# Kernel optimization log

Measured on AMD Instinct MI355X. Metric: run time of the kernel, lower is better.

## Reference

```python
import jax, jax.numpy as jnp
import numpy as np


def setup_inputs() -> dict:
    key = jax.random.key(0)
    k1, k2, k3, k4 = jax.random.split(key, 4)
    B, N, F, H, O = 4, 2048, 256, 8, 256
    nodes = jax.random.normal(k1, (B, N, F), dtype=jnp.float32)
    W_heads = jax.random.normal(k2, (H, F, F), dtype=jnp.float32) * (1.0 / np.sqrt(F))
    W_out = jax.random.normal(k3, (H * F, O), dtype=jnp.float32) * (1.0 / np.sqrt(H * F))
    bias = jax.random.normal(k4, (O,), dtype=jnp.float32) * 0.02
    return {"nodes": nodes, "W_heads": W_heads, "W_out": W_out, "bias": bias}


def reference(nodes, W_heads, W_out, bias):
    # nodes: [B,N,F]; W_heads: [H,F,F]; W_out: [H*F,O]; bias: [O]
    B, N, F = nodes.shape
    H = W_heads.shape[0]
    norm = 1.0 / jnp.sqrt(jnp.asarray(F, dtype=nodes.dtype))
    # per-head bilinear scores: (x @ W_h) @ x^T  -> [B,H,N,N]
    xw = jnp.einsum('bnf,hfg->bhng', nodes, W_heads)
    scores = jnp.einsum('bhng,bmg->bhnm', xw, nodes) * norm
    att = jax.nn.softmax(scores, axis=-1)
    # messages: att @ x (V = input nodes) -> [B,H,N,F]
    msgs = jnp.einsum('bhnm,bmf->bhnf', att, nodes)
    # concat heads along feature axis (head 0 first) -> [B,N,H*F]
    msgs = msgs.transpose(0, 2, 1, 3).reshape(B, N, H * F)
    return jnp.matmul(msgs, W_out) + bias
```

## Files before the change

kernel.cpp:

```cpp
#include <hip/hip_runtime.h>
#include <hip/hip_bf16.h>

#define B_ 4
#define N_ 2048
#define F_ 256
#define H_ 8
#define O_ 256

#define SCALE_QK 0.09016844005556021f

typedef __attribute__((ext_vector_type(8))) short short8;
typedef __attribute__((ext_vector_type(4))) short s16x4;
typedef __attribute__((ext_vector_type(4))) float f32x4;
typedef __attribute__((ext_vector_type(4))) unsigned int u32x4;

static __device__ __forceinline__ float bf2f(short u) {
    unsigned int x = ((unsigned int)(unsigned short)u) << 16;
    return __builtin_bit_cast(float, x);
}
static __device__ __forceinline__ short f2bf(float f) {
    unsigned int x = __builtin_bit_cast(unsigned int, f);
    unsigned int lsb = (x >> 16) & 1u;
    x += 0x7fffu + lsb;
    return (short)(x >> 16);
}
static __device__ __forceinline__ unsigned int cvtpk(float a, float b) {
    unsigned int r;
    asm("v_cvt_pk_bf16_f32 %0, %1, %2" : "=v"(r) : "v"(a), "v"(b));
    return r;
}

static __device__ __forceinline__ void gld16(const short* g, short* l) {
    __builtin_amdgcn_global_load_lds(
        (const __attribute__((address_space(1))) void*)g,
        (__attribute__((address_space(3))) void*)l, 16, 0, 0);
}

__global__ __launch_bounds__(256) void cvtT_kernel(const float* __restrict__ src,
                                                   short* __restrict__ dstT,
                                                   short* __restrict__ dst2,
                                                   int R, int C) {
    __shared__ short tile[32][33];
    src  += (size_t)blockIdx.z * R * C;
    dstT += (size_t)blockIdx.z * R * C;
    if (dst2) dst2 += (size_t)blockIdx.z * R * C;
    int tx = threadIdx.x, ty = threadIdx.y;
    int c0 = blockIdx.x * 32, r0 = blockIdx.y * 32;
#pragma unroll
    for (int j = 0; j < 4; j++) {
        int r = r0 + ty + j * 8;
        short v = f2bf(src[(size_t)r * C + c0 + tx]);
        tile[ty + j * 8][tx] = v;
        if (dst2) dst2[(size_t)r * C + c0 + tx] = v;
    }
    __syncthreads();
#pragma unroll
    for (int j = 0; j < 4; j++) {
        int c = c0 + ty + j * 8;
        dstT[(size_t)c * R + r0 + tx] = tile[tx][ty + j * 8];
    }
}

__global__ __launch_bounds__(512) void out_kernel(const short* __restrict__ msgs,
                                                  const short* __restrict__ WoutT,
                                                  const float* __restrict__ bias,
                                                  float* __restrict__ out) {
    __shared__ short sA[2][64 * 64];
    __shared__ short sB[2][128 * 64];
    int mt = blockIdx.x, nt = blockIdx.y;
    int tid = threadIdx.x, w = tid >> 6, l = tid & 63, lq = l & 15, quad = l >> 4;
    const short* Arow = msgs  + (size_t)(mt * 64)  * (H_ * F_);
    const short* Brow = WoutT + (size_t)(nt * 128) * (H_ * F_);
    int xk = (l & 7) ^ (l >> 3);

    f32x4 acc[4];
#pragma unroll
    for (int i = 0; i < 4; i++) acc[i] = (f32x4)(0.f);

#define STAGE_OUT(KB, BI) do {                                               \
        gld16(&Arow[(size_t)(w * 8 + (l >> 3)) * (H_ * F_) + (KB) * 64 + xk * 8], \
              &sA[BI][w * 8 * 64]);                                          \
        gld16(&Brow[(size_t)(w * 16 + (l >> 3)) * (H_ * F_) + (KB) * 64 + xk * 8], \
              &sB[BI][w * 16 * 64]);                                         \
        gld16(&Brow[(size_t)(w * 16 + 8 + (l >> 3)) * (H_ * F_) + (KB) * 64 + xk * 8], \
              &sB[BI][(w * 16 + 8) * 64]);                                   \
    } while (0)

    STAGE_OUT(0, 0);
    __syncthreads();

#pragma unroll 1
    for (int kb = 0; kb < 32; kb++) {
        int cur = kb & 1;
        if (kb < 31) STAGE_OUT(kb + 1, cur ^ 1);
        int arow = (w & 3) * 16 + lq;
#pragma unroll
        for (int kk = 0; kk < 2; kk++) {
            short8 af = *(const short8*)&sA[cur][arow * 64 + (((kk * 4 + quad) ^ (arow & 7)) * 8)];
#pragma unroll
            for (int ct = 0; ct < 4; ct++) {
                int brow = (w >> 2) * 64 + ct * 16 + lq;
                short8 bf = *(const short8*)&sB[cur][brow * 64 + (((kk * 4 + quad) ^ (brow & 7)) * 8)];
                acc[ct] = __builtin_amdgcn_mfma_f32_16x16x32_bf16(af, bf, acc[ct], 0, 0, 0);
            }
        }
        __syncthreads();
    }

#pragma unroll
    for (int ct = 0; ct < 4; ct++) {
        int gcol = nt * 128 + (w >> 2) * 64 + ct * 16 + lq;
        float bv = bias[gcol];
#pragma unroll
        for (int r = 0; r < 4; r++) {
            int row = mt * 64 + (w & 3) * 16 + quad * 4 + r;
            out[(size_t)row * O_ + gcol] = acc[ct][r] + bv;
        }
    }
}


#define STAGE_KV(KT, KVF, KVTF) do {                                         \
    _Pragma("unroll")                                                        \
    for (int i_ = 0; i_ < 4; i_++) {                                         \
        int rk_ = w * 8 + i_ * 2 + (l >> 5);                                 \
        int bk_ = (l & 31) ^ (rk_ & 31);                                     \
        gld16(&Xb[(size_t)((KT) * 64 + rk_) * F_ + bk_ * 8],                 \
              &KVF[(w * 8 + i_ * 2) * 256]);                                 \
        int rt_ = w * 32 + i_ * 8 + (l >> 3);                                \
        int bt_ = (l & 7) ^ (rt_ & 7);                                       \
        gld16(&XTb[(size_t)rt_ * N_ + (KT) * 64 + bt_ * 8],                  \
              &KVTF[(w * 32 + i_ * 8) * 64]);                                \
    }                                                                        \
} while (0)

#define COMPUTE_KT(KVF, KVTF) do {                                           \
    f32x4 sacc[4];                                                           \
    _Pragma("unroll")                                                        \
    for (int ct = 0; ct < 4; ct++) sacc[ct] = (f32x4)(0.f);                  \
    __builtin_amdgcn_s_setprio(1);                                           \
    _Pragma("unroll")                                                        \
    for (int kk = 0; kk < 8; kk++) {                                         \
        _Pragma("unroll")                                                    \
        for (int ct = 0; ct < 4; ct++) {                                     \
            int arow = ct * 16 + lq;                                         \
            int ab = (kk * 4 + quad) ^ (arow & 31);                          \
            short8 af = *(const short8*)&KVF[arow * 256 + ab * 8];           \
            sacc[ct] = __builtin_amdgcn_mfma_f32_16x16x32_bf16(af, aq[kk], sacc[ct], 0, 0, 0); \
        }                                                                    \
    }                                                                        \
    __builtin_amdgcn_s_setprio(0);                                           \
    float mx = -INFINITY;                                                    \
    _Pragma("unroll")                                                        \
    for (int ct = 0; ct < 4; ct++)                                           \
        _Pragma("unroll")                                                    \
        for (int r_ = 0; r_ < 4; r_++) mx = fmaxf(mx, sacc[ct][r_]);         \
    mx = fmaxf(mx, __shfl_xor(mx, 16));                                      \
    mx = fmaxf(mx, __shfl_xor(mx, 32));                                      \
    if (!__all(mx - m_q <= 8.0f)) {                \
        float mn = fmaxf(m_q, mx);                                           \
        float alpha = exp2f(m_q - mn);                                       \
        m_q = mn;                                                            \
        l_q *= alpha;                                                        \
        _Pragma("unroll")                                                    \
        for (int ct = 0; ct < 16; ct++)                                      \
            _Pragma("unroll")                                                \
            for (int r_ = 0; r_ < 4; r_++) oacc[ct][r_] *= alpha;            \
    }                                                                        \
    float pv[4][4]; float s_ = 0.f;                                          \
    _Pragma("unroll")                                                        \
    for (int ct = 0; ct < 4; ct++)                                           \
        _Pragma("unroll")                                                    \
        for (int r_ = 0; r_ < 4; r_++) {                                     \
            pv[ct][r_] = exp2f(sacc[ct][r_] - m_q);                          \
            s_ += pv[ct][r_];                                                \
        }                                                                    \
    s_ += __shfl_xor(s_, 16);                                                \
    s_ += __shfl_xor(s_, 32);                                                \
    l_q += s_;                                                               \
    unsigned int w2[4][2];                                                   \
    _Pragma("unroll")                                                        \
    for (int ct = 0; ct < 4; ct++) {                                         \
        w2[ct][0] = cvtpk(pv[ct][0], pv[ct][1]);                             \
        w2[ct][1] = cvtpk(pv[ct][2], pv[ct][3]);                             \
    }                                                                        \
    int sl0 = (2 * (quad & 1)) * 16 + lq;                                    \
    int sl1 = sl0 + 16;                                                      \
    bool hi = (quad >> 1) != 0;                                              \
    short8 pfrag[2];                                                         \
    _Pragma("unroll")                                                        \
    for (int kk = 0; kk < 2; kk++) {                                         \
        unsigned int u0 = __shfl((int)w2[2 * kk][0], sl0);                   \
        unsigned int u1 = __shfl((int)w2[2 * kk][1], sl0);                   \
        unsigned int u2 = __shfl((int)w2[2 * kk][0], sl1);                   \
        unsigned int u3 = __shfl((int)w2[2 * kk][1], sl1);                   \
        unsigned int v0 = __shfl((int)w2[2 * kk + 1][0], sl0);               \
        unsigned int v1 = __shfl((int)w2[2 * kk + 1][1], sl0);               \
        unsigned int v2 = __shfl((int)w2[2 * kk + 1][0], sl1);               \
        unsigned int v3 = __shfl((int)w2[2 * kk + 1][1], sl1);               \
        u32x4 pk = { hi ? v0 : u0, hi ? v1 : u1, hi ? v2 : u2, hi ? v3 : u3 }; \
        pfrag[kk] = __builtin_bit_cast(short8, pk);                          \
    }                                                                        \
    __builtin_amdgcn_s_setprio(1);                                           \
    _Pragma("unroll")                                                        \
    for (int ct = 0; ct < 16; ct++) {                                        \
        int arow = ct * 16 + lq;                                             \
        short8 a0 = *(const short8*)&KVTF[arow * 64 + ((quad) ^ (arow & 7)) * 8]; \
        short8 a1 = *(const short8*)&KVTF[arow * 64 + ((4 + quad) ^ (arow & 7)) * 8]; \
        oacc[ct] = __builtin_amdgcn_mfma_f32_16x16x32_bf16(a0, pfrag[0], oacc[ct], 0, 0, 0); \
        oacc[ct] = __builtin_amdgcn_mfma_f32_16x16x32_bf16(a1, pfrag[1], oacc[ct], 0, 0, 0); \
    }                                                                        \
    __builtin_amdgcn_s_setprio(0);                                           \
} while (0)

__global__ __launch_bounds__(512) void attn_kernel(const short* __restrict__ X,
                                                   const short* __restrict__ WhT,
                                                   const short* __restrict__ XT,
                                                   short* __restrict__ msgs) {
    __shared__ short kvfA[64 * 256];
    __shared__ short kvfB[64 * 256];
    __shared__ short kvTfA[256 * 64];
    __shared__ short kvTfB[256 * 64];

    int qt = blockIdx.x, bh = blockIdx.y, b = bh >> 3, h = bh & 7;
    int tid = threadIdx.x, w = tid >> 6, l = tid & 63, lq = l & 15, quad = l >> 4;
    int q0 = qt * 128;

    const short* Xb  = X  + (size_t)b * N_ * F_;
    const short* XTb = XT + (size_t)b * F_ * N_;
    const short* Whh = WhT + (size_t)h * F_ * F_;

    f32x4 oacc[16];
    short8 aq[8];

#pragma unroll
    for (int i = 0; i < 16; i++) oacc[i] = (f32x4)(0.f);
    {
        short* xdst = (w < 4) ? kvfA : kvfB;
        int wl = w & 3;
#pragma unroll
        for (int i = 0; i < 8; i++) {
            int r = wl * 16 + i * 2 + (l >> 5);
            int bb = (l & 31) ^ (r & 31);
            gld16(&Xb[(size_t)(q0 + ((w >> 2) * 64) + r) * F_ + bb * 8],
                  &xdst[(wl * 16 + i * 2) * 256]);
        }
    }
    const short* xsrc = (w < 4) ? kvfA : kvfB;
#pragma unroll 1
    for (int kb = 0; kb < 4; kb++) {
        __syncthreads();
#pragma unroll
        for (int i = 0; i < 4; i++) {
            int rt = w * 32 + i * 8 + (l >> 3);
            int bt = (l & 7) ^ (rt & 7);
            gld16(&Whh[(size_t)rt * F_ + kb * 64 + bt * 8], &kvTfA[(w * 32 + i * 8) * 64]);
        }
        __syncthreads();
#pragma unroll
        for (int kk = 0; kk < 2; kk++) {
            int arow = (w & 3) * 16 + lq;
            int ab = (kb * 8 + kk * 4 + quad) ^ (arow & 31);
            short8 af = *(const short8*)&xsrc[arow * 256 + ab * 8];
#pragma unroll
            for (int ct = 0; ct < 16; ct++) {
                int brow = ct * 16 + lq;
                int bb = (kk * 4 + quad) ^ (brow & 7);
                short8 bf = *(const short8*)&kvTfA[brow * 64 + bb * 8];
                oacc[ct] = __builtin_amdgcn_mfma_f32_16x16x32_bf16(af, bf, oacc[ct], 0, 0, 0);
            }
        }
    }
    __syncthreads();
    {
        short* qdst = (w < 4) ? kvTfA : kvTfB;
#pragma unroll
        for (int ct = 0; ct < 16; ct++) {
#pragma unroll
            for (int r = 0; r < 4; r++) {
                int row = (w & 3) * 16 + quad * 4 + r;
                int col = ct * 16 + lq;
                int pb = (col >> 3) ^ (row & 31);
                qdst[row * 256 + pb * 8 + (col & 7)] = f2bf(oacc[ct][r] * SCALE_QK);
            }
        }
        __syncthreads();
#pragma unroll
        for (int kk = 0; kk < 8; kk++) {
            int row = (w & 3) * 16 + lq;
            int ab = (kk * 4 + quad) ^ (row & 31);
            aq[kk] = *(const short8*)&qdst[row * 256 + ab * 8];
        }
    }
    __syncthreads();

#pragma unroll
    for (int i = 0; i < 16; i++) oacc[i] = (f32x4)(0.f);
    float m_q = -INFINITY, l_q = 0.f;

    STAGE_KV(0, kvfA, kvTfA);
    __syncthreads();

#pragma unroll 1
    for (int kt2 = 0; kt2 < 16; kt2++) {
        STAGE_KV(2 * kt2 + 1, kvfB, kvTfB);
        COMPUTE_KT(kvfA, kvTfA);
        __syncthreads();
        STAGE_KV((2 * kt2 + 2) & 31, kvfA, kvTfA);
        COMPUTE_KT(kvfB, kvTfB);
        __syncthreads();
    }

    float inv = 1.f / l_q;
    short* Mout = msgs + (size_t)(b * N_ + q0 + w * 16 + lq) * (H_ * F_) + h * F_;
#pragma unroll
    for (int ct = 0; ct < 16; ct++) {
        s16x4 v4 = { f2bf(oacc[ct][0] * inv), f2bf(oacc[ct][1] * inv),
                     f2bf(oacc[ct][2] * inv), f2bf(oacc[ct][3] * inv) };
        *(s16x4*)&Mout[ct * 16 + quad * 4] = v4;
    }
}

extern "C" void kernel_launch(void* const* d_in, const int* in_sizes, int n_in,
                              void* d_out, int out_size, void* d_ws, size_t ws_size,
                              hipStream_t stream) {
    const float* nodes = (const float*)d_in[0];
    const float* Wh    = (const float*)d_in[1];
    const float* Wout  = (const float*)d_in[2];
    const float* bias  = (const float*)d_in[3];
    float* out = (float*)d_out;

    char* ws = (char*)d_ws;
    short* msgs   = (short*)(ws);
    short* WhT    = (short*)(ws + 33554432);
    short* WoutT  = (short*)(ws + 34603008);
    short* XT     = (short*)(ws + 35651584);
    short* Xbf    = (short*)(ws + 39845888);

    dim3 tblk(32, 8, 1);
    hipLaunchKernelGGL(cvtT_kernel, dim3(8, 8, 8),  tblk, 0, stream, Wh,    WhT,   (short*)nullptr, 256,  256);
    hipLaunchKernelGGL(cvtT_kernel, dim3(8, 64, 1), tblk, 0, stream, Wout,  WoutT, (short*)nullptr, 2048, 256);
    hipLaunchKernelGGL(cvtT_kernel, dim3(8, 64, 4), tblk, 0, stream, nodes, XT,    Xbf,             2048, 256);

    hipLaunchKernelGGL(attn_kernel, dim3(16, 32), dim3(512), 0, stream, Xbf, WhT, XT, msgs);
    hipLaunchKernelGGL(out_kernel,  dim3(128, 2), dim3(512), 0, stream, msgs, WoutT, bias, out);
}
```

Before: 289.0 us.

## Double attention block to 16 waves covering 256 query rows per workgroup

```diff
diff --git a/kernel.cpp b/kernel.cpp
--- a/kernel.cpp
+++ b/kernel.cpp
@@ -122,15 +122,15 @@
 
 #define STAGE_KV(KT, KVF, KVTF) do {                                         \
     _Pragma("unroll")                                                        \
-    for (int i_ = 0; i_ < 4; i_++) {                                         \
-        int rk_ = w * 8 + i_ * 2 + (l >> 5);                                 \
+    for (int i_ = 0; i_ < 2; i_++) {                                         \
+        int rk_ = w * 4 + i_ * 2 + (l >> 5);                                 \
         int bk_ = (l & 31) ^ (rk_ & 31);                                     \
         gld16(&Xb[(size_t)((KT) * 64 + rk_) * F_ + bk_ * 8],                 \
-              &KVF[(w * 8 + i_ * 2) * 256]);                                 \
-        int rt_ = w * 32 + i_ * 8 + (l >> 3);                                \
+              &KVF[(w * 4 + i_ * 2) * 256]);                                 \
+        int rt_ = w * 16 + i_ * 8 + (l >> 3);                                \
         int bt_ = (l & 7) ^ (rt_ & 7);                                       \
         gld16(&XTb[(size_t)rt_ * N_ + (KT) * 64 + bt_ * 8],                  \
-              &KVTF[(w * 32 + i_ * 8) * 64]);                                \
+              &KVTF[(w * 16 + i_ * 8) * 64]);                                \
     }                                                                        \
 } while (0)
 
@@ -213,10 +213,10 @@
     __builtin_amdgcn_s_setprio(0);                                           \
 } while (0)
 
-__global__ __launch_bounds__(512) void attn_kernel(const short* __restrict__ X,
-                                                   const short* __restrict__ WhT,
-                                                   const short* __restrict__ XT,
-                                                   short* __restrict__ msgs) {
+__global__ __launch_bounds__(1024) void attn_kernel(const short* __restrict__ X,
+                                                    const short* __restrict__ WhT,
+                                                    const short* __restrict__ XT,
+                                                    short* __restrict__ msgs) {
     __shared__ short kvfA[64 * 256];
     __shared__ short kvfB[64 * 256];
     __shared__ short kvTfA[256 * 64];
@@ -224,7 +224,9 @@
 
     int qt = blockIdx.x, bh = blockIdx.y, b = bh >> 3, h = bh & 7;
     int tid = threadIdx.x, w = tid >> 6, l = tid & 63, lq = l & 15, quad = l >> 4;
-    int q0 = qt * 128;
+    int q0 = qt * 256;
+    int g = w & 7;
+    int fh = w >> 3;
 
     const short* Xb  = X  + (size_t)b * N_ * F_;
     const short* XTb = XT + (size_t)b * F_ * N_;
@@ -233,63 +235,68 @@
     f32x4 oacc[16];
     short8 aq[8];
 
-#pragma unroll
-    for (int i = 0; i < 16; i++) oacc[i] = (f32x4)(0.f);
-    {
-        short* xdst = (w < 4) ? kvfA : kvfB;
-        int wl = w & 3;
-#pragma unroll
-        for (int i = 0; i < 8; i++) {
-            int r = wl * 16 + i * 2 + (l >> 5);
-            int bb = (l & 31) ^ (r & 31);
-            gld16(&Xb[(size_t)(q0 + ((w >> 2) * 64) + r) * F_ + bb * 8],
-                  &xdst[(wl * 16 + i * 2) * 256]);
-        }
-    }
-    const short* xsrc = (w < 4) ? kvfA : kvfB;
 #pragma unroll 1
-    for (int kb = 0; kb < 4; kb++) {
+    for (int hp = 0; hp < 2; hp++) {
+        {
+            short* xdst = (w < 8) ? kvfA : kvfB;
+#pragma unroll
+            for (int i = 0; i < 4; i++) {
+                int rl = g * 8 + i * 2 + (l >> 5);
+                int bb = (l & 31) ^ (rl & 31);
+                gld16(&Xb[(size_t)(q0 + hp * 128 + fh * 64 + rl) * F_ + bb * 8],
+                      &xdst[(g * 8 + i * 2) * 256]);
+            }
+        }
+#pragma unroll
+        for (int i = 0; i < 8; i++) oacc[i] = (f32x4)(0.f);
+        const short* xsrc = (g < 4) ? kvfA : kvfB;
+        int arowl = (g & 3) * 16 + lq;
+#pragma unroll 1
+        for (int kb = 0; kb < 4; kb++) {
+            __syncthreads();
+#pragma unroll
+            for (int i = 0; i < 2; i++) {
+                int rt = w * 16 + i * 8 + (l >> 3);
+                int bt = (l & 7) ^ (rt & 7);
+                gld16(&Whh[(size_t)rt * F_ + kb * 64 + bt * 8], &kvTfA[(w * 16 + i * 8) * 64]);
+            }
+            __syncthreads();
+#pragma unroll
+            for (int kk = 0; kk < 2; kk++) {
+                int ab = (kb * 8 + kk * 4 + quad) ^ (arowl & 31);
+                short8 af = *(const short8*)&xsrc[arowl * 256 + ab * 8];
+#pragma unroll
+                for (int ct = 0; ct < 8; ct++) {
+                    int brow = fh * 128 + ct * 16 + lq;
+                    int bb = (kk * 4 + quad) ^ (brow & 7);
+                    short8 bf = *(const short8*)&kvTfA[brow * 64 + bb * 8];
+                    oacc[ct] = __builtin_amdgcn_mfma_f32_16x16x32_bf16(af, bf, oacc[ct], 0, 0, 0);
+                }
+            }
+        }
         __syncthreads();
-#pragma unroll
-        for (int i = 0; i < 4; i++) {
-            int rt = w * 32 + i * 8 + (l >> 3);
-            int bt = (l & 7) ^ (rt & 7);
-            gld16(&Whh[(size_t)rt * F_ + kb * 64 + bt * 8], &kvTfA[(w * 32 + i * 8) * 64]);
-        }
-        __syncthreads();
-#pragma unroll
-        for (int kk = 0; kk < 2; kk++) {
-            int arow = (w & 3) * 16 + lq;
-            int ab = (kb * 8 + kk * 4 + quad) ^ (arow & 31);
-            short8 af = *(const short8*)&xsrc[arow * 256 + ab * 8];
-#pragma unroll
-            for (int ct = 0; ct < 16; ct++) {
-                int brow = ct * 16 + lq;
-                int bb = (kk * 4 + quad) ^ (brow & 7);
-                short8 bf = *(const short8*)&kvTfA[brow * 64 + bb * 8];
-                oacc[ct] = __builtin_amdgcn_mfma_f32_16x16x32_bf16(af, bf, oacc[ct], 0, 0, 0);
-            }
-        }
-    }
-    __syncthreads();
-    {
-        short* qdst = (w < 4) ? kvTfA : kvTfB;
-#pragma unroll
-        for (int ct = 0; ct < 16; ct++) {
-#pragma unroll
-            for (int r = 0; r < 4; r++) {
-                int row = (w & 3) * 16 + quad * 4 + r;
-                int col = ct * 16 + lq;
-                int pb = (col >> 3) ^ (row & 31);
-                qdst[row * 256 + pb * 8 + (col & 7)] = f2bf(oacc[ct][r] * SCALE_QK);
-            }
-        }
-        __syncthreads();
-#pragma unroll
-        for (int kk = 0; kk < 8; kk++) {
-            int row = (w & 3) * 16 + lq;
-            int ab = (kk * 4 + quad) ^ (row & 31);
-            aq[kk] = *(const short8*)&qdst[row * 256 + ab * 8];
+        {
+            short* qdst = (g < 4) ? kvTfA : kvTfB;
+#pragma unroll
+            for (int ct = 0; ct < 8; ct++) {
+#pragma unroll
+                for (int r = 0; r < 4; r++) {
+                    int rl = (g & 3) * 16 + quad * 4 + r;
+                    int col = fh * 128 + ct * 16 + lq;
+                    int pb = (col >> 3) ^ (rl & 31);
+                    qdst[rl * 256 + pb * 8 + (col & 7)] = f2bf(oacc[ct][r] * SCALE_QK);
+                }
+            }
+            __syncthreads();
+            if (fh == hp) {
+                const short* qsrc = (g < 4) ? kvTfA : kvTfB;
+                int rl = (g & 3) * 16 + lq;
+#pragma unroll
+                for (int kk = 0; kk < 8; kk++) {
+                    int ab = (kk * 4 + quad) ^ (rl & 31);
+                    aq[kk] = *(const short8*)&qsrc[rl * 256 + ab * 8];
+                }
+            }
         }
     }
     __syncthreads();
@@ -342,6 +349,6 @@
     hipLaunchKernelGGL(cvtT_kernel, dim3(8, 64, 1), tblk, 0, stream, Wout,  WoutT, (short*)nullptr, 2048, 256);
     hipLaunchKernelGGL(cvtT_kernel, dim3(8, 64, 4), tblk, 0, stream, nodes, XT,    Xbf,             2048, 256);
 
-    hipLaunchKernelGGL(attn_kernel, dim3(16, 32), dim3(512), 0, stream, Xbf, WhT, XT, msgs);
+    hipLaunchKernelGGL(attn_kernel, dim3(8, 32), dim3(1024), 0, stream, Xbf, WhT, XT, msgs);
     hipLaunchKernelGGL(out_kernel,  dim3(128, 2), dim3(512), 0, stream, msgs, WoutT, bias, out);
 }
```

Result: slower. 437.6 us (+51.4%).
